# Kernel optimization log

Measured on AMD Instinct MI355X. Metric: run time of the kernel, lower is better.

## Reference

```python
import jax, jax.numpy as jnp
import numpy as np

N_NODES = 100000
N_EDGES = 800000
NODE_F = 32
EDGE_F = 16
HID = 128
EPS = 1e-5


def _bn(h, g, b):
    # BatchNorm1d in training mode: biased batch stats over dim 0
    m = h.mean(axis=0)
    v = jnp.mean((h - m) ** 2, axis=0)
    return (h - m) * jax.lax.rsqrt(v + EPS) * g + b


def _sage(x, src, dst, Wl, bl, Wr):
    # PyG SAGEConv (mean aggr): lin_l(mean_{j->i} x_j) + lin_r(x_i)
    s = jax.ops.segment_sum(x[src], dst, num_segments=N_NODES)
    cnt = jax.ops.segment_sum(jnp.ones((src.shape[0], 1), x.dtype), dst, num_segments=N_NODES)
    mean = s / jnp.maximum(cnt, 1.0)
    return mean @ Wl + bl + x @ Wr


def setup_inputs() -> dict:
    key = jax.random.key(0)
    ks = jax.random.split(key, 32)

    def lin(k, fi, fo):
        return jax.random.normal(k, (fi, fo), jnp.float32) / np.sqrt(fi)

    inp = {
        'x': jax.random.normal(ks[0], (N_NODES, NODE_F), jnp.float32),
        'edge_index': jax.random.randint(ks[1], (2, N_EDGES), 0, N_NODES),
        'edge_attr': jax.random.normal(ks[2], (N_EDGES, EDGE_F), jnp.float32),
        'edge_source': jax.random.randint(ks[3], (N_EDGES,), 0, N_NODES),
        'edge_target': jax.random.randint(ks[4], (N_EDGES,), 0, N_NODES),
        'W1l': lin(ks[5], NODE_F, HID), 'b1': jnp.zeros((HID,), jnp.float32), 'W1r': lin(ks[6], NODE_F, HID),
        'W2l': lin(ks[7], HID, HID), 'b2': jnp.zeros((HID,), jnp.float32), 'W2r': lin(ks[8], HID, HID),
        'bn1_g': jnp.ones((HID,), jnp.float32), 'bn1_b': jnp.zeros((HID,), jnp.float32),
        'bn2_g': jnp.ones((HID,), jnp.float32), 'bn2_b': jnp.zeros((HID,), jnp.float32),
        'We': lin(ks[9], EDGE_F, HID), 'be': jnp.zeros((HID,), jnp.float32),
        'bne_g': jnp.ones((HID,), jnp.float32), 'bne_b': jnp.zeros((HID,), jnp.float32),
        'Wm1': lin(ks[10], 3 * HID, HID), 'bm1': jnp.zeros((HID,), jnp.float32),
        'bnm_g': jnp.ones((HID,), jnp.float32), 'bnm_b': jnp.zeros((HID,), jnp.float32),
        'Wm2': lin(ks[11], HID, HID // 2), 'bm2': jnp.zeros((HID // 2,), jnp.float32),
        'Wm3': lin(ks[12], HID // 2, 1), 'bm3': jnp.zeros((1,), jnp.float32),
    }
    return inp


def reference(x, edge_index, edge_attr, edge_source, edge_target,
              W1l, b1, W1r, W2l, b2, W2r, bn1_g, bn1_b, bn2_g, bn2_b,
              We, be, bne_g, bne_b, Wm1, bm1, bnm_g, bnm_b, Wm2, bm2, Wm3, bm3):
    src, dst = edge_index[0], edge_index[1]
    h = jax.nn.relu(_bn(_sage(x, src, dst, W1l, b1, W1r), bn1_g, bn1_b))  # dropout = identity (eval)
    h = jax.nn.relu(_bn(_sage(h, src, dst, W2l, b2, W2r), bn2_g, bn2_b))
    ef = _bn(jax.nn.relu(edge_attr @ We + be), bne_g, bne_b)  # Linear->ReLU->BN->Dropout(id)
    z = jnp.concatenate([h[edge_source], h[edge_target], ef], axis=1)  # [E, 3*HID]
    z = _bn(jax.nn.relu(z @ Wm1 + bm1), bnm_g, bnm_b)
    z = jax.nn.relu(z @ Wm2 + bm2)
    return (z @ Wm3 + bm3).squeeze(-1)
```

## Files before the change

kernel.cpp:

```cpp
#include <hip/hip_runtime.h>
#include <hip/hip_bf16.h>

#define NN 100000
#define NE 800000
#define SCAN_NB 98

typedef __attribute__((ext_vector_type(8))) short bf16x8;
typedef __attribute__((ext_vector_type(4))) float f32x4;

__device__ __forceinline__ short f2b(float f) {
    unsigned u = __float_as_uint(f);
    unsigned r = (u + 0x7fffu + ((u >> 16) & 1u)) >> 16;
    return (short)r;
}
__device__ __forceinline__ float b2f(short s) {
    return __uint_as_float(((unsigned)(unsigned short)s) << 16);
}

__global__ __launch_bounds__(256) void k_hist(const int* __restrict__ ei, int* __restrict__ deg)
{
    int e = blockIdx.x * 256 + threadIdx.x;
    if (e < NE) atomicAdd(&deg[ei[NE + e]], 1);
}

__global__ __launch_bounds__(1024) void k_scan_a(const int* __restrict__ deg,
    int* __restrict__ tmp, int* __restrict__ bsum)
{
    __shared__ int sh[1024];
    int t = threadIdx.x, b = blockIdx.x;
    int idx = b * 1024 + t;
    int v = (idx < NN) ? deg[idx] : 0;
    sh[t] = v;
    __syncthreads();
    for (int ofs = 1; ofs < 1024; ofs <<= 1) {
        int u = (t >= ofs) ? sh[t - ofs] : 0;
        __syncthreads();
        sh[t] += u;
        __syncthreads();
    }
    if (idx < NN) tmp[idx] = sh[t] - v;
    if (t == 1023) bsum[b] = sh[1023];
}

__global__ void k_scan_b(const int* __restrict__ bsum, int* __restrict__ boff,
    int* __restrict__ rowptr)
{
    if (threadIdx.x == 0) {
        int acc = 0;
        for (int i = 0; i < SCAN_NB; i++) { boff[i] = acc; acc += bsum[i]; }
        rowptr[NN] = acc;
    }
}

__global__ __launch_bounds__(1024) void k_scan_c(const int* __restrict__ tmp,
    const int* __restrict__ boff, int* __restrict__ rowptr, int* __restrict__ wp)
{
    int b = blockIdx.x, t = threadIdx.x;
    int idx = b * 1024 + t;
    if (idx < NN) {
        int v = boff[b] + tmp[idx];
        rowptr[idx] = v; wp[idx] = v;
    }
}

__global__ __launch_bounds__(256) void k_scatter(const int* __restrict__ ei,
    int* __restrict__ wp, int* __restrict__ elist)
{
    int e = blockIdx.x * 256 + threadIdx.x;
    if (e < NE) {
        int d = ei[NE + e];
        int pos = atomicAdd(&wp[d], 1);
        elist[pos] = ei[e];
    }
}

__global__ __launch_bounds__(256) void k_gagg1(const float* __restrict__ x,
    const int* __restrict__ rowptr, const int* __restrict__ elist, float* __restrict__ meanX)
{
    int n = blockIdx.x * 8 + (threadIdx.x >> 5);
    int j = threadIdx.x & 31;
    int b = rowptr[n], e = rowptr[n + 1];
    float acc = 0.f;
    for (int i = b; i < e; i++) {
        int s = elist[i];
        acc += x[(size_t)s * 32 + j];
    }
    float inv = (e > b) ? 1.0f / (float)(e - b) : 1.0f;
    meanX[(size_t)n * 32 + j] = acc * inv;
}

__global__ __launch_bounds__(256) void k_gagg2(const short* __restrict__ h1b,
    const int* __restrict__ rowptr, const int* __restrict__ elist,
    const float* __restrict__ sc1, const float* __restrict__ sh1, short* __restrict__ m2b)
{
    int n = blockIdx.x * 8 + (threadIdx.x >> 5);
    int c0 = (threadIdx.x & 31) * 4;
    float sc[4], sh[4];
    #pragma unroll
    for (int i = 0; i < 4; i++) { sc[i] = sc1[c0 + i]; sh[i] = sh1[c0 + i]; }
    int b = rowptr[n], e = rowptr[n + 1];
    float acc[4] = {0.f, 0.f, 0.f, 0.f};
    for (int i = b; i < e; i++) {
        int s = elist[i];
        ushort4 u = *(const ushort4*)(h1b + (size_t)s * 128 + c0);
        acc[0] += fmaxf(b2f((short)u.x) * sc[0] + sh[0], 0.f);
        acc[1] += fmaxf(b2f((short)u.y) * sc[1] + sh[1], 0.f);
        acc[2] += fmaxf(b2f((short)u.z) * sc[2] + sh[2], 0.f);
        acc[3] += fmaxf(b2f((short)u.w) * sc[3] + sh[3], 0.f);
    }
    float inv = (e > b) ? 1.0f / (float)(e - b) : 1.0f;
    ushort4 o;
    o.x = (unsigned short)f2b(acc[0] * inv);
    o.y = (unsigned short)f2b(acc[1] * inv);
    o.z = (unsigned short)f2b(acc[2] * inv);
    o.w = (unsigned short)f2b(acc[3] * inv);
    *(ushort4*)(m2b + (size_t)n * 128 + c0) = o;
}

__global__ __launch_bounds__(256) void k_node_l1(
    const float* __restrict__ meanX, const float* __restrict__ x,
    const float* __restrict__ Wl, const float* __restrict__ Wr,
    const float* __restrict__ bias,
    short* __restrict__ outp, float* __restrict__ ssum, float* __restrict__ ssq)
{
    __shared__ __align__(16) float sWl[32][128];
    __shared__ __align__(16) float sWr[32][128];
    __shared__ __align__(16) float sA[32][36];
    __shared__ __align__(16) float sB[32][36];
    __shared__ float red[2][128], red2[2][128];
    int tid = threadIdx.x;
    int j = tid & 127, rg = tid >> 7;
    int r0 = blockIdx.x * 32;

    for (int f = tid * 4; f < 4096; f += 1024) {
        *(float4*)((float*)sWl + f) = *(const float4*)(Wl + f);
        *(float4*)((float*)sWr + f) = *(const float4*)(Wr + f);
    }
    {
        int r = tid >> 3, c = (tid & 7) * 4;
        *(float4*)(&sA[r][c]) = *(const float4*)(meanX + (size_t)(r0 + r) * 32 + c);
        *(float4*)(&sB[r][c]) = *(const float4*)(x + (size_t)(r0 + r) * 32 + c);
    }
    __syncthreads();

    float acc[16];
    #pragma unroll
    for (int r = 0; r < 16; r++) acc[r] = 0.0f;
    int rb = rg * 16;
    #pragma unroll
    for (int kq = 0; kq < 8; kq++) {
        int k = kq * 4;
        float wl0 = sWl[k][j], wl1 = sWl[k+1][j], wl2 = sWl[k+2][j], wl3 = sWl[k+3][j];
        float wr0 = sWr[k][j], wr1 = sWr[k+1][j], wr2 = sWr[k+2][j], wr3 = sWr[k+3][j];
        #pragma unroll
        for (int r = 0; r < 16; r++) {
            float4 a = *(float4*)(&sA[rb + r][k]);
            float4 b = *(float4*)(&sB[rb + r][k]);
            acc[r] += a.x*wl0 + a.y*wl1 + a.z*wl2 + a.w*wl3
                    + b.x*wr0 + b.y*wr1 + b.z*wr2 + b.w*wr3;
        }
    }
    float bj = bias[j];
    float s1 = 0.0f, s2 = 0.0f;
    #pragma unroll
    for (int r = 0; r < 16; r++) {
        float v = acc[r] + bj;
        outp[(size_t)(r0 + rb + r) * 128 + j] = f2b(v);
        s1 += v; s2 += v * v;
    }
    red[rg][j] = s1; red2[rg][j] = s2;
    __syncthreads();
    if (rg == 0) {
        atomicAdd(&ssum[j], red[0][j] + red[1][j]);
        atomicAdd(&ssq[j],  red2[0][j] + red2[1][j]);
    }
}

__global__ __launch_bounds__(256) void k_node_l2m(
    const short* __restrict__ m2b, const short* __restrict__ h1b,
    const float* __restrict__ sc1, const float* __restrict__ sh1,
    const short* __restrict__ W2cT, const float* __restrict__ bias,
    short* __restrict__ h2b, float* __restrict__ ssum, float* __restrict__ ssq)
{
    __shared__ __align__(16) short sK[32][264];
    __shared__ float sRed[2][128];
    __shared__ float sS[128], sH[128];
    const int tid = threadIdx.x;
    const int wave = tid >> 6, lane = tid & 63, quad = lane >> 4, ln = lane & 15;
    const int waveM = wave >> 1, waveN = wave & 1;
    const int colbase = 64 * waveN, row16 = 16 * waveM;
    if (tid < 128) { sS[tid] = sc1[tid]; sH[tid] = sh1[tid]; sRed[0][tid] = 0.f; sRed[1][tid] = 0.f; }

    bf16x8 bW[4][8];
    #pragma unroll
    for (int nt = 0; nt < 4; nt++)
        #pragma unroll
        for (int kk = 0; kk < 8; kk++)
            bW[nt][kk] = *(const bf16x8*)(W2cT + (size_t)(colbase + nt * 16 + ln) * 256 + kk * 32 + quad * 8);
    float bc[4];
    #pragma unroll
    for (int nt = 0; nt < 4; nt++) bc[nt] = bias[colbase + nt * 16 + ln];

    float s1[4] = {0,0,0,0}, s2[4] = {0,0,0,0};
    f32x4 zero = {0.f, 0.f, 0.f, 0.f};
    __syncthreads();

    for (int t = blockIdx.x; t < NN / 32; t += gridDim.x) {
        int r0 = t * 32;
        __syncthreads();
        {
            int r = tid >> 3, seg = tid & 7;
            if (seg < 4) {
                const bf16x8* src = (const bf16x8*)(m2b + (size_t)(r0 + r) * 128 + seg * 32);
                bf16x8* dst = (bf16x8*)(&sK[r][seg * 32]);
                dst[0] = src[0]; dst[1] = src[1]; dst[2] = src[2]; dst[3] = src[3];
            } else {
                int c0 = (seg - 4) * 32;
                const short* src = h1b + (size_t)(r0 + r) * 128 + c0;
                short tmp[32];
                #pragma unroll
                for (int i = 0; i < 32; i++)
                    tmp[i] = f2b(fmaxf(b2f(src[i]) * sS[c0 + i] + sH[c0 + i], 0.f));
                bf16x8* dst = (bf16x8*)(&sK[r][128 + c0]);
                dst[0] = *(bf16x8*)(tmp); dst[1] = *(bf16x8*)(tmp + 8);
                dst[2] = *(bf16x8*)(tmp + 16); dst[3] = *(bf16x8*)(tmp + 24);
            }
        }
        __syncthreads();
        f32x4 acc[4] = {zero, zero, zero, zero};
        #pragma unroll
        for (int kk = 0; kk < 8; kk++) {
            bf16x8 a = *(const bf16x8*)(&sK[row16 + ln][kk * 32 + quad * 8]);
            #pragma unroll
            for (int nt = 0; nt < 4; nt++)
                acc[nt] = __builtin_amdgcn_mfma_f32_16x16x32_bf16(a, bW[nt][kk], acc[nt], 0, 0, 0);
        }
        #pragma unroll
        for (int nt = 0; nt < 4; nt++) {
            int col = colbase + nt * 16 + ln;
            #pragma unroll
            for (int r = 0; r < 4; r++) {
                float v = acc[nt][r] + bc[nt];
                h2b[(size_t)(r0 + row16 + quad * 4 + r) * 128 + col] = f2b(v);
                s1[nt] += v; s2[nt] += v * v;
            }
        }
    }
    #pragma unroll
    for (int nt = 0; nt < 4; nt++) {
        float a1 = s1[nt], a2 = s2[nt];
        a1 += __shfl_down(a1, 32); a1 += __shfl_down(a1, 16);
        a2 += __shfl_down(a2, 32); a2 += __shfl_down(a2, 16);
        if (quad == 0) {
            atomicAdd(&sRed[0][colbase + nt * 16 + ln], a1);
            atomicAdd(&sRed[1][colbase + nt * 16 + ln], a2);
        }
    }
    __syncthreads();
    if (tid < 128) {
        atomicAdd(&ssum[tid], sRed[0][tid]);
        atomicAdd(&ssq[tid],  sRed[1][tid]);
    }
}

__global__ void k_bn_fin(const float* __restrict__ ssum, const float* __restrict__ ssq,
    const float* __restrict__ g, const float* __restrict__ b, float count,
    float* __restrict__ scale, float* __restrict__ shift)
{
    int j = threadIdx.x;
    float m = ssum[j] / count;
    float var = ssq[j] / count - m * m;
    float rs = rsqrtf(var + 1e-5f);
    float sc = g[j] * rs;
    scale[j] = sc;
    shift[j] = b[j] - m * sc;
}

__global__ void k_prep(const float* __restrict__ We, const float* __restrict__ Wm1,
                       const float* __restrict__ W2l, const float* __restrict__ W2r,
                       short* __restrict__ WteT, short* __restrict__ WmsT,
                       short* __restrict__ WmdT, short* __restrict__ W2cT)
{
    int j = threadIdx.x;
    int b = blockIdx.x;
    if (b == 0) {
        for (int k = 0; k < 32; k++)
            WteT[j * 32 + k] = (k < 16) ? f2b(We[k * 128 + j]) : (short)0;
    } else if (b == 1) {
        for (int k = 0; k < 128; k++) WmsT[j * 128 + k] = f2b(Wm1[k * 128 + j]);
    } else if (b == 2) {
        for (int k = 0; k < 128; k++) WmdT[j * 128 + k] = f2b(Wm1[(128 + k) * 128 + j]);
    } else if (b == 3) {
        for (int k = 0; k < 128; k++) W2cT[j * 256 + k] = f2b(W2l[k * 128 + j]);
    } else {
        for (int k = 0; k < 128; k++) W2cT[j * 256 + 128 + k] = f2b(W2r[k * 128 + j]);
    }
}

__global__ void k_fold_e(const float* __restrict__ ssum, const float* __restrict__ ssq,
    const float* __restrict__ g, const float* __restrict__ b,
    const float* __restrict__ Wm1, const float* __restrict__ bm1,
    short* __restrict__ W1pT, float* __restrict__ bm1p)
{
    __shared__ float sa[128], sc[128];
    int tid = threadIdx.x;
    float m = ssum[tid] / (float)NE;
    float var = ssq[tid] / (float)NE - m * m;
    float rs = rsqrtf(var + 1e-5f);
    float a = g[tid] * rs;
    sa[tid] = a; sc[tid] = b[tid] - m * a;
    __syncthreads();
    float acc = bm1[tid];
    for (int k = 0; k < 128; k++) {
        float w = Wm1[(256 + k) * 128 + tid];
        W1pT[tid * 128 + k] = f2b(sa[k] * w);
        acc += sc[k] * w;
    }
    bm1p[tid] = acc;
}

__global__ void k_fold_m(const float* __restrict__ ssum, const float* __restrict__ ssq,
    const float* __restrict__ g, const float* __restrict__ b,
    const float* __restrict__ Wm2, const float* __restrict__ bm2,
    short* __restrict__ W2pT, float* __restrict__ b2p)
{
    __shared__ float sa[128], sc[128];
    int tid = threadIdx.x;
    float m = ssum[tid] / (float)NE;
    float var = ssq[tid] / (float)NE - m * m;
    float rs = rsqrtf(var + 1e-5f);
    float a = g[tid] * rs;
    sa[tid] = a; sc[tid] = b[tid] - m * a;
    __syncthreads();
    if (tid < 64) {
        float acc = bm2[tid];
        for (int k = 0; k < 128; k++) {
            float w = Wm2[k * 64 + tid];
            W2pT[tid * 128 + k] = f2b(sa[k] * w);
            acc += sc[k] * w;
        }
        b2p[tid] = acc;
    }
}

__global__ __launch_bounds__(256) void k_proj_mfma(
    const short* __restrict__ h2b, const float* __restrict__ sc2, const float* __restrict__ sh2,
    const short* __restrict__ WT0, const short* __restrict__ WT1,
    short* __restrict__ C0, short* __restrict__ C1)
{
    __shared__ __align__(16) short sA[32][136];
    __shared__ float sS[128], sH[128];
    const int tid = threadIdx.x;
    const int wave = tid >> 6, lane = tid & 63, quad = lane >> 4, ln = lane & 15;
    const int waveM = wave >> 1, waveN = wave & 1;
    const int colbase = 64 * waveN, row16 = 16 * waveM;
    const int half = (blockIdx.x >= 640) ? 1 : 0;
    const short* WT = half ? WT1 : WT0;
    short* C = half ? C1 : C0;
    const int b0 = blockIdx.x - half * 640;
    if (tid < 128) { sS[tid] = sc2[tid]; sH[tid] = sh2[tid]; }
    bf16x8 bW[4][4];
    #pragma unroll
    for (int nt = 0; nt < 4; nt++)
        #pragma unroll
        for (int kk = 0; kk < 4; kk++)
            bW[nt][kk] = *(const bf16x8*)(WT + (colbase + nt * 16 + ln) * 128 + kk * 32 + quad * 8);
    f32x4 zero = {0.f, 0.f, 0.f, 0.f};
    __syncthreads();
    for (int t = b0; t < NN / 32; t += 640) {
        int r0 = t * 32;
        __syncthreads();
        {
            int r = tid >> 3, c0 = (tid & 7) * 16;
            const short* p = h2b + (size_t)(r0 + r) * 128 + c0;
            short tmp[16];
            #pragma unroll
            for (int i = 0; i < 16; i++)
                tmp[i] = f2b(fmaxf(b2f(p[i]) * sS[c0 + i] + sH[c0 + i], 0.f));
            *(bf16x8*)(&sA[r][c0])     = *(bf16x8*)tmp;
            *(bf16x8*)(&sA[r][c0 + 8]) = *(bf16x8*)(tmp + 8);
        }
        __syncthreads();
        f32x4 acc[4] = {zero, zero, zero, zero};
        #pragma unroll
        for (int kk = 0; kk < 4; kk++) {
            bf16x8 a = *(const bf16x8*)(&sA[row16 + ln][kk * 32 + quad * 8]);
            #pragma unroll
            for (int nt = 0; nt < 4; nt++)
                acc[nt] = __builtin_amdgcn_mfma_f32_16x16x32_bf16(a, bW[nt][kk], acc[nt], 0, 0, 0);
        }
        #pragma unroll
        for (int nt = 0; nt < 4; nt++) {
            int col = colbase + nt * 16 + ln;
            #pragma unroll
            for (int r = 0; r < 4; r++)
                C[(size_t)(r0 + row16 + quad * 4 + r) * 128 + col] = f2b(acc[nt][r]);
        }
    }
}

template<int MODE, bool STOREV = false>
__global__ __launch_bounds__(256) void k_edge_mfma(
    const float* __restrict__ ea,
    const short* __restrict__ WteT, const float* __restrict__ be,
    const short* __restrict__ W1pT, const float* __restrict__ bm1p,
    const short* __restrict__ hs, const short* __restrict__ hd,
    const int* __restrict__ esrc, const int* __restrict__ etgt,
    const short* __restrict__ W2pT, const float* __restrict__ b2p,
    const float* __restrict__ Wm3, const float* __restrict__ bm3,
    float* __restrict__ ssum, float* __restrict__ ssq,
    short* __restrict__ vbuf, float* __restrict__ outp)
{
    __shared__ __align__(16) short sT[32][136];
    __shared__ __align__(16) float sSum[32][132];
    __shared__ float sRed[2][128];
    __shared__ __align__(16) short sW2[64][136];
    __shared__ float sZ[32][69];
    __shared__ float sW3[64];

    const int tid = threadIdx.x;
    const int wave = tid >> 6, lane = tid & 63;
    const int quad = lane >> 4, ln = lane & 15;
    const int waveM = wave >> 1, waveN = wave & 1;
    const int colbase = 64 * waveN, row16 = 16 * waveM;

    if (MODE < 2) {
        if (tid < 128) { sRed[0][tid] = 0.f; sRed[1][tid] = 0.f; }
    }
    if (MODE >= 2) {
        int q = tid >> 2, kb = (tid & 3) * 32;
        const bf16x8* src = (const bf16x8*)(W2pT + q * 128 + kb);
        bf16x8* dst = (bf16x8*)(&sW2[q][kb]);
        dst[0] = src[0]; dst[1] = src[1]; dst[2] = src[2]; dst[3] = src[3];
        if (tid < 64) sW3[tid] = Wm3[tid];
    }

    bf16x8 bWe[4], bW1[4][4];
    if (MODE <= 2) {
        #pragma unroll
        for (int nt = 0; nt < 4; nt++) {
            bWe[nt] = *(const bf16x8*)(WteT + (colbase + nt * 16 + ln) * 32 + quad * 8);
            if (MODE >= 1) {
                #pragma unroll
                for (int kk = 0; kk < 4; kk++)
                    bW1[nt][kk] = *(const bf16x8*)(W1pT + (colbase + nt * 16 + ln) * 128 + kk * 32 + quad * 8);
            }
        }
    }
    float bec[4], bmc[4];
    #pragma unroll
    for (int nt = 0; nt < 4; nt++) {
        bec[nt] = (MODE <= 2) ? be[colbase + nt * 16 + ln] : 0.f;
        bmc[nt] = (MODE == 1 || MODE == 2) ? bm1p[colbase + nt * 16 + ln] : 0.f;
    }
    float b2c[2] = {0.f, 0.f};
    if (MODE >= 2) { b2c[0] = b2p[32 * waveN + ln]; b2c[1] = b2p[32 * waveN + 16 + ln]; }
    float bm3v = (MODE >= 2) ? bm3[0] : 0.f;

    const int srow = tid >> 4;
    const int scol = (tid & 15) * 8;

    float s1[4] = {0,0,0,0}, s2[4] = {0,0,0,0};
    f32x4 zero = {0.f, 0.f, 0.f, 0.f};
    __syncthreads();

    if constexpr (MODE == 1) {
        const int G = gridDim.x;
        const int NT = NE / 32;
        bf16x8 gA = {}, gB = {}, gC = {}, gD = {};
        int i1sA = 0, i1tA = 0, i1sB = 0, i1tB = 0;
        float4 fe0 = {0,0,0,0}, fe1 = {0,0,0,0};

        int t = blockIdx.x;
        if (t < NT) {
            const int e0 = t * 32;
            int s0 = esrc[e0 + srow],      q0 = etgt[e0 + srow];
            int s1i = esrc[e0 + srow + 16], q1 = etgt[e0 + srow + 16];
            gA = *(const bf16x8*)(hs + (size_t)s0 * 128 + scol);
            gB = *(const bf16x8*)(hd + (size_t)q0 * 128 + scol);
            gC = *(const bf16x8*)(hs + (size_t)s1i * 128 + scol);
            gD = *(const bf16x8*)(hd + (size_t)q1 * 128 + scol);
            int t1 = t + G;
            if (t1 < NT) {
                const int e1 = t1 * 32;
                i1sA = esrc[e1 + srow];      i1tA = etgt[e1 + srow];
                i1sB = esrc[e1 + srow + 16]; i1tB = etgt[e1 + srow + 16];
            }
            if (quad < 2) {
                const float* p = ea + (size_t)(e0 + row16 + ln) * 16 + quad * 8;
                fe0 = *(const float4*)p; fe1 = *(const float4*)(p + 4);
            }
        }

        for (; t < NT; t += G) {
            const int e0 = t * 32;

            bf16x8 aE;
            #pragma unroll
            for (int i = 0; i < 8; i++) aE[i] = 0;
            if (quad < 2) {
                aE[0]=f2b(fe0.x); aE[1]=f2b(fe0.y); aE[2]=f2b(fe0.z); aE[3]=f2b(fe0.w);
                aE[4]=f2b(fe1.x); aE[5]=f2b(fe1.y); aE[6]=f2b(fe1.z); aE[7]=f2b(fe1.w);
            }
            f32x4 tacc[4];
            #pragma unroll
            for (int nt = 0; nt < 4; nt++)
                tacc[nt] = __builtin_amdgcn_mfma_f32_16x16x32_bf16(aE, bWe[nt], zero, 0, 0, 0);

            __syncthreads();

            #pragma unroll
            for (int nt = 0; nt < 4; nt++) {
                int col = colbase + nt * 16 + ln;
                #pragma unroll
                for (int r = 0; r < 4; r++)
                    sT[row16 + quad * 4 + r][col] = f2b(fmaxf(tacc[nt][r] + bec[nt], 0.f));
            }
            {
                f32x4 a0, a1, b0, b1;
                #pragma unroll
                for (int i = 0; i < 4; i++) {
                    a0[i] = b2f(gA[i])     + b2f(gB[i]);
                    a1[i] = b2f(gA[i + 4]) + b2f(gB[i + 4]);
                    b0[i] = b2f(gC[i])     + b2f(gD[i]);
                    b1[i] = b2f(gC[i + 4]) + b2f(gD[i + 4]);
                }
                *(f32x4*)(&sSum[srow][scol])          = a0;
                *(f32x4*)(&sSum[srow][scol + 4])      = a1;
                *(f32x4*)(&sSum[srow + 16][scol])     = b0;
                *(f32x4*)(&sSum[srow + 16][scol + 4]) = b1;
            }
            {
                int t1 = t + G;
                if (t1 < NT) {
                    gA = *(const bf16x8*)(hs + (size_t)i1sA * 128 + scol);
                    gB = *(const bf16x8*)(hd + (size_t)i1tA * 128 + scol);
                    gC = *(const bf16x8*)(hs + (size_t)i1sB * 128 + scol);
                    gD = *(const bf16x8*)(hd + (size_t)i1tB * 128 + scol);
                    int t2 = t1 + G;
                    if (t2 < NT) {
                        const int e2 = t2 * 32;
                        i1sA = esrc[e2 + srow];      i1tA = etgt[e2 + srow];
                        i1sB = esrc[e2 + srow + 16]; i1tB = etgt[e2 + srow + 16];
                    }
                    if (quad < 2) {
                        const float* p = ea + (size_t)(t1 * 32 + row16 + ln) * 16 + quad * 8;
                        fe0 = *(const float4*)p; fe1 = *(const float4*)(p + 4);
                    }
                }
            }
            __syncthreads();

            f32x4 uacc[4] = {zero, zero, zero, zero};
            #pragma unroll
            for (int kk = 0; kk < 4; kk++) {
                bf16x8 aU = *(const bf16x8*)(&sT[row16 + ln][kk * 32 + quad * 8]);
                #pragma unroll
                for (int nt = 0; nt < 4; nt++)
                    uacc[nt] = __builtin_amdgcn_mfma_f32_16x16x32_bf16(aU, bW1[nt][kk], uacc[nt], 0, 0, 0);
            }
            #pragma unroll
            for (int nt = 0; nt < 4; nt++) {
                int col = colbase + nt * 16 + ln;
                #pragma unroll
                for (int r = 0; r < 4; r++) {
                    float v = uacc[nt][r] + bmc[nt] + sSum[row16 + quad * 4 + r][col];
                    v = fmaxf(v, 0.f);
                    s1[nt] += v; s2[nt] += v * v;
                    if constexpr (STOREV)
                        vbuf[(size_t)(e0 + row16 + quad * 4 + r) * 128 + col] = f2b(v);
                }
            }
        }
    } else {

    for (int t = blockIdx.x; t < NE / 32; t += gridDim.x) {
        const int e0 = t * 32;

        if (MODE == 3) {
            f32x4 vacc[2] = {zero, zero};
            #pragma unroll
            for (int kk = 0; kk < 4; kk++) {
                bf16x8 aV = *(const bf16x8*)(vbuf + (size_t)(e0 + row16 + ln) * 128 + kk * 32 + quad * 8);
                #pragma unroll
                for (int n2 = 0; n2 < 2; n2++) {
                    bf16x8 bV = *(const bf16x8*)(&sW2[32 * waveN + n2 * 16 + ln][kk * 32 + quad * 8]);
                    vacc[n2] = __builtin_amdgcn_mfma_f32_16x16x32_bf16(aV, bV, vacc[n2], 0, 0, 0);
                }
            }
            __syncthreads();
            #pragma unroll
            for (int n2 = 0; n2 < 2; n2++) {
                int col2 = 32 * waveN + n2 * 16 + ln;
                #pragma unroll
                for (int r = 0; r < 4; r++)
                    sZ[row16 + quad * 4 + r][col2] = fmaxf(vacc[n2][r] + b2c[n2], 0.f);
            }
            __syncthreads();
            {
                int row = wave * 8 + (lane >> 3);
                int ks  = (lane & 7) * 8;
                float o = 0.f;
                #pragma unroll
                for (int k2 = 0; k2 < 8; k2++)
                    o += sZ[row][ks + k2] * sW3[ks + k2];
                o += __shfl_xor(o, 1);
                o += __shfl_xor(o, 2);
                o += __shfl_xor(o, 4);
                if ((lane & 7) == 0) outp[e0 + row] = o + bm3v;
            }
            continue;
        }

        int isA = 0, itA = 0, isB = 0, itB = 0;
        if (MODE == 2) {
            isA = esrc[e0 + srow];      itA = etgt[e0 + srow];
            isB = esrc[e0 + srow + 16]; itB = etgt[e0 + srow + 16];
        }

        bf16x8 aE;
        #pragma unroll
        for (int i = 0; i < 8; i++) aE[i] = 0;
        if (quad < 2) {
            const float* p = ea + (size_t)(e0 + row16 + ln) * 16 + quad * 8;
            float4 f0 = *(const float4*)p, f1 = *(const float4*)(p + 4);
            aE[0]=f2b(f0.x); aE[1]=f2b(f0.y); aE[2]=f2b(f0.z); aE[3]=f2b(f0.w);
            aE[4]=f2b(f1.x); aE[5]=f2b(f1.y); aE[6]=f2b(f1.z); aE[7]=f2b(f1.w);
        }
        f32x4 tacc[4];
        #pragma unroll
        for (int nt = 0; nt < 4; nt++)
            tacc[nt] = __builtin_amdgcn_mfma_f32_16x16x32_bf16(aE, bWe[nt], zero, 0, 0, 0);

        if (MODE == 0) {
            #pragma unroll
            for (int nt = 0; nt < 4; nt++)
                #pragma unroll
                for (int r = 0; r < 4; r++) {
                    float v = fmaxf(tacc[nt][r] + bec[nt], 0.f);
                    s1[nt] += v; s2[nt] += v * v;
                }
            continue;
        }

        __syncthreads();
        {
            bf16x8 gA = *(const bf16x8*)(hs + (size_t)isA * 128 + scol);
            bf16x8 gB = *(const bf16x8*)(hd + (size_t)itA * 128 + scol);
            bf16x8 gC = *(const bf16x8*)(hs + (size_t)isB * 128 + scol);
            bf16x8 gD = *(const bf16x8*)(hd + (size_t)itB * 128 + scol);
            #pragma unroll
            for (int nt = 0; nt < 4; nt++) {
                int col = colbase + nt * 16 + ln;
                #pragma unroll
                for (int r = 0; r < 4; r++)
                    sT[row16 + quad * 4 + r][col] = f2b(fmaxf(tacc[nt][r] + bec[nt], 0.f));
            }
            f32x4 a0, a1, b0, b1;
            #pragma unroll
            for (int i = 0; i < 4; i++) {
                a0[i] = b2f(gA[i])     + b2f(gB[i]);
                a1[i] = b2f(gA[i + 4]) + b2f(gB[i + 4]);
                b0[i] = b2f(gC[i])     + b2f(gD[i]);
                b1[i] = b2f(gC[i + 4]) + b2f(gD[i + 4]);
            }
            *(f32x4*)(&sSum[srow][scol])          = a0;
            *(f32x4*)(&sSum[srow][scol + 4])      = a1;
            *(f32x4*)(&sSum[srow + 16][scol])     = b0;
            *(f32x4*)(&sSum[srow + 16][scol + 4]) = b1;
        }
        __syncthreads();

        f32x4 uacc[4] = {zero, zero, zero, zero};
        #pragma unroll
        for (int kk = 0; kk < 4; kk++) {
            bf16x8 aU = *(const bf16x8*)(&sT[row16 + ln][kk * 32 + quad * 8]);
            #pragma unroll
            for (int nt = 0; nt < 4; nt++)
                uacc[nt] = __builtin_amdgcn_mfma_f32_16x16x32_bf16(aU, bW1[nt][kk], uacc[nt], 0, 0, 0);
        }

        {
            __syncthreads();
            #pragma unroll
            for (int nt = 0; nt < 4; nt++) {
                int col = colbase + nt * 16 + ln;
                #pragma unroll
                for (int r = 0; r < 4; r++) {
                    float v = uacc[nt][r] + bmc[nt] + sSum[row16 + quad * 4 + r][col];
                    sT[row16 + quad * 4 + r][col] = f2b(fmaxf(v, 0.f));
                }
            }
            __syncthreads();
            f32x4 vacc[2] = {zero, zero};
            #pragma unroll
            for (int kk = 0; kk < 4; kk++) {
                bf16x8 aV = *(const bf16x8*)(&sT[row16 + ln][kk * 32 + quad * 8]);
                #pragma unroll
                for (int n2 = 0; n2 < 2; n2++) {
                    bf16x8 bV = *(const bf16x8*)(&sW2[32 * waveN + n2 * 16 + ln][kk * 32 + quad * 8]);
                    vacc[n2] = __builtin_amdgcn_mfma_f32_16x16x32_bf16(aV, bV, vacc[n2], 0, 0, 0);
                }
            }
            #pragma unroll
            for (int n2 = 0; n2 < 2; n2++) {
                int col2 = 32 * waveN + n2 * 16 + ln;
                #pragma unroll
                for (int r = 0; r < 4; r++)
                    sZ[row16 + quad * 4 + r][col2] = fmaxf(vacc[n2][r] + b2c[n2], 0.f);
            }
            __syncthreads();
            {
                int row = wave * 8 + (lane >> 3);
                int ks  = (lane & 7) * 8;
                float o = 0.f;
                #pragma unroll
                for (int k2 = 0; k2 < 8; k2++)
                    o += sZ[row][ks + k2] * sW3[ks + k2];
                o += __shfl_xor(o, 1);
                o += __shfl_xor(o, 2);
                o += __shfl_xor(o, 4);
                if ((lane & 7) == 0) outp[e0 + row] = o + bm3v;
            }
        }
    }

    }

    if (MODE < 2) {
        #pragma unroll
        for (int nt = 0; nt < 4; nt++) {
            float a1 = s1[nt], a2 = s2[nt];
            a1 += __shfl_down(a1, 32); a1 += __shfl_down(a1, 16);
            a2 += __shfl_down(a2, 32); a2 += __shfl_down(a2, 16);
            if (quad == 0) {
                atomicAdd(&sRed[0][colbase + nt * 16 + ln], a1);
                atomicAdd(&sRed[1][colbase + nt * 16 + ln], a2);
            }
        }
        __syncthreads();
        if (tid < 128) {
            atomicAdd(&ssum[tid], sRed[0][tid]);
            atomicAdd(&ssq[tid],  sRed[1][tid]);
        }
    }
}

extern "C" void kernel_launch(void* const* d_in, const int* in_sizes, int n_in,
                              void* d_out, int out_size, void* d_ws, size_t ws_size,
                              hipStream_t stream) {
    const float* x     = (const float*)d_in[0];
    const int*   ei    = (const int*)  d_in[1];
    const float* eattr = (const float*)d_in[2];
    const int*   esrc  = (const int*)  d_in[3];
    const int*   etgt  = (const int*)  d_in[4];
    const float* W1l = (const float*)d_in[5];  const float* b1 = (const float*)d_in[6];
    const float* W1r = (const float*)d_in[7];
    const float* W2l = (const float*)d_in[8];  const float* b2 = (const float*)d_in[9];
    const float* W2r = (const float*)d_in[10];
    const float* bn1_g = (const float*)d_in[11]; const float* bn1_b = (const float*)d_in[12];
    const float* bn2_g = (const float*)d_in[13]; const float* bn2_b = (const float*)d_in[14];
    const float* We  = (const float*)d_in[15]; const float* be  = (const float*)d_in[16];
    const float* bne_g = (const float*)d_in[17]; const float* bne_b = (const float*)d_in[18];
    const float* Wm1 = (const float*)d_in[19]; const float* bm1 = (const float*)d_in[20];
    const float* bnm_g = (const float*)d_in[21]; const float* bnm_b = (const float*)d_in[22];
    const float* Wm2 = (const float*)d_in[23]; const float* bm2 = (const float*)d_in[24];
    const float* Wm3 = (const float*)d_in[25]; const float* bm3 = (const float*)d_in[26];
    float* out = (float*)d_out;

    char* base = (char*)d_ws;
    size_t o = 0;
    auto A = [&](size_t bytes) { char* p = base + o; o = (o + bytes + 255) & ~(size_t)255; return p; };
    short* hsb   = (short*)A((size_t)NN * 128 * 2);
    short* hdb   = (short*)A((size_t)NN * 128 * 2);
    int*   deg   = (int*)  A((size_t)NN * 4);
    int*   rowptr= (int*)  A((size_t)(NN + 1) * 4);
    int*   wp    = (int*)  A((size_t)NN * 4);
    int*   elist = (int*)  A((size_t)NE * 4);
    float* st    = (float*)A(1024 * 4);
    int*   bsum  = (int*)  A(SCAN_NB * 4);
    int*   boff  = (int*)  A(SCAN_NB * 4);
    float* sc1   = (float*)A(512); float* sh1 = (float*)A(512);
    float* sc2   = (float*)A(512); float* sh2 = (float*)A(512);
    float* bm1p  = (float*)A(512); float* b2p = (float*)A(256);
    short* WteT  = (short*)A(128 * 32 * 2);
    short* W1pT  = (short*)A(128 * 128 * 2);
    short* WmsT  = (short*)A(128 * 128 * 2);
    short* WmdT  = (short*)A(128 * 128 * 2);
    short* W2pT  = (short*)A(64 * 128 * 2);
    short* W2cT  = (short*)A(128 * 256 * 2);
    size_t chain = o;
    float* meanX = (float*)A((size_t)NN * 32 * 4);
    short* h1b   = (short*)A((size_t)NN * 128 * 2);
    short* m2b   = (short*)A((size_t)NN * 128 * 2);
    short* h2b   = (short*)A((size_t)NN * 128 * 2);
    int*   stmp  = (int*)meanX;
    short* vbuf  = (short*)(base + chain);
    bool storev = ws_size >= chain + (size_t)NE * 128 * 2;

    hipMemsetAsync(deg, 0, (size_t)NN * 4, stream);
    hipMemsetAsync(st, 0, 1024 * 4, stream);

    k_prep<<<5, 128, 0, stream>>>(We, Wm1, W2l, W2r, WteT, WmsT, WmdT, W2cT);
    k_hist<<<(NE + 255) / 256, 256, 0, stream>>>(ei, deg);
    k_scan_a<<<SCAN_NB, 1024, 0, stream>>>(deg, stmp, bsum);
    k_scan_b<<<1, 64, 0, stream>>>(bsum, boff, rowptr);
    k_scan_c<<<SCAN_NB, 1024, 0, stream>>>(stmp, boff, rowptr, wp);
    k_scatter<<<(NE + 255) / 256, 256, 0, stream>>>(ei, wp, elist);

    k_edge_mfma<0><<<1024, 256, 0, stream>>>(eattr, WteT, be, W1pT, bm1p, hsb, hdb,
        esrc, etgt, W2pT, b2p, Wm3, bm3, st + 512, st + 640, nullptr, out);
    k_fold_e<<<1, 128, 0, stream>>>(st + 512, st + 640, bne_g, bne_b, Wm1, bm1, W1pT, bm1p);

    k_gagg1<<<NN / 8, 256, 0, stream>>>(x, rowptr, elist, meanX);
    k_node_l1<<<NN / 32, 256, 0, stream>>>(meanX, x, W1l, W1r, b1, h1b, st + 0, st + 128);
    k_bn_fin<<<1, 128, 0, stream>>>(st + 0, st + 128, bn1_g, bn1_b, (float)NN, sc1, sh1);

    k_gagg2<<<NN / 8, 256, 0, stream>>>(h1b, rowptr, elist, sc1, sh1, m2b);
    k_node_l2m<<<640, 256, 0, stream>>>(m2b, h1b, sc1, sh1, W2cT, b2, h2b, st + 256, st + 384);
    k_bn_fin<<<1, 128, 0, stream>>>(st + 256, st + 384, bn2_g, bn2_b, (float)NN, sc2, sh2);

    k_proj_mfma<<<1280, 256, 0, stream>>>(h2b, sc2, sh2, WmsT, WmdT, hsb, hdb);

    if (storev)
        k_edge_mfma<1, true><<<1280, 256, 0, stream>>>(eattr, WteT, be, W1pT, bm1p, hsb, hdb,
            esrc, etgt, W2pT, b2p, Wm3, bm3, st + 768, st + 896, vbuf, out);
    else
        k_edge_mfma<1, false><<<1280, 256, 0, stream>>>(eattr, WteT, be, W1pT, bm1p, hsb, hdb,
            esrc, etgt, W2pT, b2p, Wm3, bm3, st + 768, st + 896, nullptr, out);
    k_fold_m<<<1, 128, 0, stream>>>(st + 768, st + 896, bnm_g, bnm_b, Wm2, bm2, W2pT, b2p);

    if (storev)
        k_edge_mfma<3><<<2048, 256, 0, stream>>>(eattr, WteT, be, W1pT, bm1p, hsb, hdb,
            esrc, etgt, W2pT, b2p, Wm3, bm3, nullptr, nullptr, vbuf, out);
    else
        k_edge_mfma<2><<<1280, 256, 0, stream>>>(eattr, WteT, be, W1pT, bm1p, hsb, hdb,
            esrc, etgt, W2pT, b2p, Wm3, bm3, nullptr, nullptr, nullptr, out);
}
```

Baseline: 813.6 us.

## Unroll gather loops, prefetch next tile in edge kernels, retune grid sizes

The neighbor-gather loops in both SAGE aggregation kernels are unrolled by four so several independent row loads are in flight at once. The edge-attribute stats pass (mode 0) and the final MLP pass over stored activations (mode 3) are split into dedicated loops that load the next tile into registers before computing the current one. Grid sizes for several kernels change, with matching stride changes in the projection kernel. This hides gather and global-load latency at the cost of more registers and a different float summation order.

```diff
diff --git a/kernel.cpp b/kernel.cpp
--- a/kernel.cpp
+++ b/kernel.cpp
@@ -81,10 +81,16 @@
     int j = threadIdx.x & 31;
     int b = rowptr[n], e = rowptr[n + 1];
     float acc = 0.f;
-    for (int i = b; i < e; i++) {
-        int s = elist[i];
-        acc += x[(size_t)s * 32 + j];
-    }
+    int i = b;
+    for (; i + 4 <= e; i += 4) {
+        int s0 = elist[i], s1 = elist[i + 1], s2 = elist[i + 2], s3 = elist[i + 3];
+        float a0 = x[(size_t)s0 * 32 + j];
+        float a1 = x[(size_t)s1 * 32 + j];
+        float a2 = x[(size_t)s2 * 32 + j];
+        float a3 = x[(size_t)s3 * 32 + j];
+        acc += (a0 + a1) + (a2 + a3);
+    }
+    for (; i < e; i++) acc += x[(size_t)elist[i] * 32 + j];
     float inv = (e > b) ? 1.0f / (float)(e - b) : 1.0f;
     meanX[(size_t)n * 32 + j] = acc * inv;
 }
@@ -100,7 +106,23 @@
     for (int i = 0; i < 4; i++) { sc[i] = sc1[c0 + i]; sh[i] = sh1[c0 + i]; }
     int b = rowptr[n], e = rowptr[n + 1];
     float acc[4] = {0.f, 0.f, 0.f, 0.f};
-    for (int i = b; i < e; i++) {
+    int i = b;
+    for (; i + 4 <= e; i += 4) {
+        int s0 = elist[i], s1 = elist[i + 1], s2 = elist[i + 2], s3 = elist[i + 3];
+        ushort4 u0 = *(const ushort4*)(h1b + (size_t)s0 * 128 + c0);
+        ushort4 u1 = *(const ushort4*)(h1b + (size_t)s1 * 128 + c0);
+        ushort4 u2 = *(const ushort4*)(h1b + (size_t)s2 * 128 + c0);
+        ushort4 u3 = *(const ushort4*)(h1b + (size_t)s3 * 128 + c0);
+        acc[0] += fmaxf(b2f((short)u0.x) * sc[0] + sh[0], 0.f) + fmaxf(b2f((short)u1.x) * sc[0] + sh[0], 0.f)
+                + fmaxf(b2f((short)u2.x) * sc[0] + sh[0], 0.f) + fmaxf(b2f((short)u3.x) * sc[0] + sh[0], 0.f);
+        acc[1] += fmaxf(b2f((short)u0.y) * sc[1] + sh[1], 0.f) + fmaxf(b2f((short)u1.y) * sc[1] + sh[1], 0.f)
+                + fmaxf(b2f((short)u2.y) * sc[1] + sh[1], 0.f) + fmaxf(b2f((short)u3.y) * sc[1] + sh[1], 0.f);
+        acc[2] += fmaxf(b2f((short)u0.z) * sc[2] + sh[2], 0.f) + fmaxf(b2f((short)u1.z) * sc[2] + sh[2], 0.f)
+                + fmaxf(b2f((short)u2.z) * sc[2] + sh[2], 0.f) + fmaxf(b2f((short)u3.z) * sc[2] + sh[2], 0.f);
+        acc[3] += fmaxf(b2f((short)u0.w) * sc[3] + sh[3], 0.f) + fmaxf(b2f((short)u1.w) * sc[3] + sh[3], 0.f)
+                + fmaxf(b2f((short)u2.w) * sc[3] + sh[3], 0.f) + fmaxf(b2f((short)u3.w) * sc[3] + sh[3], 0.f);
+    }
+    for (; i < e; i++) {
         int s = elist[i];
         ushort4 u = *(const ushort4*)(h1b + (size_t)s * 128 + c0);
         acc[0] += fmaxf(b2f((short)u.x) * sc[0] + sh[0], 0.f);
@@ -354,10 +376,10 @@
     const int wave = tid >> 6, lane = tid & 63, quad = lane >> 4, ln = lane & 15;
     const int waveM = wave >> 1, waveN = wave & 1;
     const int colbase = 64 * waveN, row16 = 16 * waveM;
-    const int half = (blockIdx.x >= 640) ? 1 : 0;
+    const int half = (blockIdx.x >= 512) ? 1 : 0;
     const short* WT = half ? WT1 : WT0;
     short* C = half ? C1 : C0;
-    const int b0 = blockIdx.x - half * 640;
+    const int b0 = blockIdx.x - half * 512;
     if (tid < 128) { sS[tid] = sc2[tid]; sH[tid] = sh2[tid]; }
     bf16x8 bW[4][4];
     #pragma unroll
@@ -367,7 +389,7 @@
             bW[nt][kk] = *(const bf16x8*)(WT + (colbase + nt * 16 + ln) * 128 + kk * 32 + quad * 8);
     f32x4 zero = {0.f, 0.f, 0.f, 0.f};
     __syncthreads();
-    for (int t = b0; t < NN / 32; t += 640) {
+    for (int t = b0; t < NN / 32; t += 512) {
         int r0 = t * 32;
         __syncthreads();
         {
@@ -572,20 +594,74 @@
                 }
             }
         }
-    } else {
-
-    for (int t = blockIdx.x; t < NE / 32; t += gridDim.x) {
-        const int e0 = t * 32;
-
-        if (MODE == 3) {
+    } else if constexpr (MODE == 0) {
+        const int G = gridDim.x;
+        const int NT = NE / 32;
+        float4 fe0 = {0,0,0,0}, fe1 = {0,0,0,0};
+        int t = blockIdx.x;
+        if (t < NT && quad < 2) {
+            const float* p = ea + (size_t)(t * 32 + row16 + ln) * 16 + quad * 8;
+            fe0 = *(const float4*)p; fe1 = *(const float4*)(p + 4);
+        }
+        for (; t < NT; t += G) {
+            bf16x8 aE;
+            #pragma unroll
+            for (int i = 0; i < 8; i++) aE[i] = 0;
+            if (quad < 2) {
+                aE[0]=f2b(fe0.x); aE[1]=f2b(fe0.y); aE[2]=f2b(fe0.z); aE[3]=f2b(fe0.w);
+                aE[4]=f2b(fe1.x); aE[5]=f2b(fe1.y); aE[6]=f2b(fe1.z); aE[7]=f2b(fe1.w);
+            }
+            int t1 = t + G;
+            if (t1 < NT && quad < 2) {
+                const float* p = ea + (size_t)(t1 * 32 + row16 + ln) * 16 + quad * 8;
+                fe0 = *(const float4*)p; fe1 = *(const float4*)(p + 4);
+            }
+            f32x4 tacc[4];
+            #pragma unroll
+            for (int nt = 0; nt < 4; nt++)
+                tacc[nt] = __builtin_amdgcn_mfma_f32_16x16x32_bf16(aE, bWe[nt], zero, 0, 0, 0);
+            #pragma unroll
+            for (int nt = 0; nt < 4; nt++)
+                #pragma unroll
+                for (int r = 0; r < 4; r++) {
+                    float v = fmaxf(tacc[nt][r] + bec[nt], 0.f);
+                    s1[nt] += v; s2[nt] += v * v;
+                }
+        }
+    } else if constexpr (MODE == 3) {
+        const int G = gridDim.x;
+        const int NT = NE / 32;
+        bf16x8 aV0 = {}, aV1 = {}, aV2 = {}, aV3 = {};
+        int t = blockIdx.x;
+        if (t < NT) {
+            const short* p = vbuf + (size_t)(t * 32 + row16 + ln) * 128 + quad * 8;
+            aV0 = *(const bf16x8*)(p);
+            aV1 = *(const bf16x8*)(p + 32);
+            aV2 = *(const bf16x8*)(p + 64);
+            aV3 = *(const bf16x8*)(p + 96);
+        }
+        for (; t < NT; t += G) {
+            const int e0 = t * 32;
             f32x4 vacc[2] = {zero, zero};
             #pragma unroll
-            for (int kk = 0; kk < 4; kk++) {
-                bf16x8 aV = *(const bf16x8*)(vbuf + (size_t)(e0 + row16 + ln) * 128 + kk * 32 + quad * 8);
-                #pragma unroll
-                for (int n2 = 0; n2 < 2; n2++) {
-                    bf16x8 bV = *(const bf16x8*)(&sW2[32 * waveN + n2 * 16 + ln][kk * 32 + quad * 8]);
-                    vacc[n2] = __builtin_amdgcn_mfma_f32_16x16x32_bf16(aV, bV, vacc[n2], 0, 0, 0);
+            for (int n2 = 0; n2 < 2; n2++) {
+                bf16x8 bV0 = *(const bf16x8*)(&sW2[32 * waveN + n2 * 16 + ln][0 * 32 + quad * 8]);
+                bf16x8 bV1 = *(const bf16x8*)(&sW2[32 * waveN + n2 * 16 + ln][1 * 32 + quad * 8]);
+                bf16x8 bV2 = *(const bf16x8*)(&sW2[32 * waveN + n2 * 16 + ln][2 * 32 + quad * 8]);
+                bf16x8 bV3 = *(const bf16x8*)(&sW2[32 * waveN + n2 * 16 + ln][3 * 32 + quad * 8]);
+                vacc[n2] = __builtin_amdgcn_mfma_f32_16x16x32_bf16(aV0, bV0, vacc[n2], 0, 0, 0);
+                vacc[n2] = __builtin_amdgcn_mfma_f32_16x16x32_bf16(aV1, bV1, vacc[n2], 0, 0, 0);
+                vacc[n2] = __builtin_amdgcn_mfma_f32_16x16x32_bf16(aV2, bV2, vacc[n2], 0, 0, 0);
+                vacc[n2] = __builtin_amdgcn_mfma_f32_16x16x32_bf16(aV3, bV3, vacc[n2], 0, 0, 0);
+            }
+            {
+                int t1 = t + G;
+                if (t1 < NT) {
+                    const short* p = vbuf + (size_t)(t1 * 32 + row16 + ln) * 128 + quad * 8;
+                    aV0 = *(const bf16x8*)(p);
+                    aV1 = *(const bf16x8*)(p + 32);
+                    aV2 = *(const bf16x8*)(p + 64);
+                    aV3 = *(const bf16x8*)(p + 96);
                 }
             }
             __syncthreads();
@@ -609,14 +685,13 @@
                 o += __shfl_xor(o, 4);
                 if ((lane & 7) == 0) outp[e0 + row] = o + bm3v;
             }
-            continue;
-        }
-
-        int isA = 0, itA = 0, isB = 0, itB = 0;
-        if (MODE == 2) {
-            isA = esrc[e0 + srow];      itA = etgt[e0 + srow];
-            isB = esrc[e0 + srow + 16]; itB = etgt[e0 + srow + 16];
-        }
+        }
+    } else {
+    for (int t = blockIdx.x; t < NE / 32; t += gridDim.x) {
+        const int e0 = t * 32;
+
+        int isA = esrc[e0 + srow],      itA = etgt[e0 + srow];
+        int isB = esrc[e0 + srow + 16], itB = etgt[e0 + srow + 16];
 
         bf16x8 aE;
         #pragma unroll
@@ -632,17 +707,6 @@
         for (int nt = 0; nt < 4; nt++)
             tacc[nt] = __builtin_amdgcn_mfma_f32_16x16x32_bf16(aE, bWe[nt], zero, 0, 0, 0);
 
-        if (MODE == 0) {
-            #pragma unroll
-            for (int nt = 0; nt < 4; nt++)
-                #pragma unroll
-                for (int r = 0; r < 4; r++) {
-                    float v = fmaxf(tacc[nt][r] + bec[nt], 0.f);
-                    s1[nt] += v; s2[nt] += v * v;
-                }
-            continue;
-        }
-
         __syncthreads();
         {
             bf16x8 gA = *(const bf16x8*)(hs + (size_t)isA * 128 + scol);
@@ -680,51 +744,48 @@
                 uacc[nt] = __builtin_amdgcn_mfma_f32_16x16x32_bf16(aU, bW1[nt][kk], uacc[nt], 0, 0, 0);
         }
 
+        __syncthreads();
+        #pragma unroll
+        for (int nt = 0; nt < 4; nt++) {
+            int col = colbase + nt * 16 + ln;
+            #pragma unroll
+            for (int r = 0; r < 4; r++) {
+                float v = uacc[nt][r] + bmc[nt] + sSum[row16 + quad * 4 + r][col];
+                sT[row16 + quad * 4 + r][col] = f2b(fmaxf(v, 0.f));
+            }
+        }
+        __syncthreads();
+        f32x4 vacc[2] = {zero, zero};
+        #pragma unroll
+        for (int kk = 0; kk < 4; kk++) {
+            bf16x8 aV = *(const bf16x8*)(&sT[row16 + ln][kk * 32 + quad * 8]);
+            #pragma unroll
+            for (int n2 = 0; n2 < 2; n2++) {
+                bf16x8 bV = *(const bf16x8*)(&sW2[32 * waveN + n2 * 16 + ln][kk * 32 + quad * 8]);
+                vacc[n2] = __builtin_amdgcn_mfma_f32_16x16x32_bf16(aV, bV, vacc[n2], 0, 0, 0);
+            }
+        }
+        #pragma unroll
+        for (int n2 = 0; n2 < 2; n2++) {
+            int col2 = 32 * waveN + n2 * 16 + ln;
+            #pragma unroll
+            for (int r = 0; r < 4; r++)
+                sZ[row16 + quad * 4 + r][col2] = fmaxf(vacc[n2][r] + b2c[n2], 0.f);
+        }
+        __syncthreads();
         {
-            __syncthreads();
-            #pragma unroll
-            for (int nt = 0; nt < 4; nt++) {
-                int col = colbase + nt * 16 + ln;
-                #pragma unroll
-                for (int r = 0; r < 4; r++) {
-                    float v = uacc[nt][r] + bmc[nt] + sSum[row16 + quad * 4 + r][col];
-                    sT[row16 + quad * 4 + r][col] = f2b(fmaxf(v, 0.f));
-                }
-            }
-            __syncthreads();
-            f32x4 vacc[2] = {zero, zero};
-            #pragma unroll
-            for (int kk = 0; kk < 4; kk++) {
-                bf16x8 aV = *(const bf16x8*)(&sT[row16 + ln][kk * 32 + quad * 8]);
-                #pragma unroll
-                for (int n2 = 0; n2 < 2; n2++) {
-                    bf16x8 bV = *(const bf16x8*)(&sW2[32 * waveN + n2 * 16 + ln][kk * 32 + quad * 8]);
-                    vacc[n2] = __builtin_amdgcn_mfma_f32_16x16x32_bf16(aV, bV, vacc[n2], 0, 0, 0);
-                }
-            }
-            #pragma unroll
-            for (int n2 = 0; n2 < 2; n2++) {
-                int col2 = 32 * waveN + n2 * 16 + ln;
-                #pragma unroll
-                for (int r = 0; r < 4; r++)
-                    sZ[row16 + quad * 4 + r][col2] = fmaxf(vacc[n2][r] + b2c[n2], 0.f);
-            }
-            __syncthreads();
-            {
-                int row = wave * 8 + (lane >> 3);
-                int ks  = (lane & 7) * 8;
-                float o = 0.f;
-                #pragma unroll
-                for (int k2 = 0; k2 < 8; k2++)
-                    o += sZ[row][ks + k2] * sW3[ks + k2];
-                o += __shfl_xor(o, 1);
-                o += __shfl_xor(o, 2);
-                o += __shfl_xor(o, 4);
-                if ((lane & 7) == 0) outp[e0 + row] = o + bm3v;
-            }
-        }
-    }
-
+            int row = wave * 8 + (lane >> 3);
+            int ks  = (lane & 7) * 8;
+            float o = 0.f;
+            #pragma unroll
+            for (int k2 = 0; k2 < 8; k2++)
+                o += sZ[row][ks + k2] * sW3[ks + k2];
+            o += __shfl_xor(o, 1);
+            o += __shfl_xor(o, 2);
+            o += __shfl_xor(o, 4);
+            if ((lane & 7) == 0) outp[e0 + row] = o + bm3v;
+        }
+    }
     }
 
     if (MODE < 2) {
@@ -808,7 +869,7 @@
     k_scan_c<<<SCAN_NB, 1024, 0, stream>>>(stmp, boff, rowptr, wp);
     k_scatter<<<(NE + 255) / 256, 256, 0, stream>>>(ei, wp, elist);
 
-    k_edge_mfma<0><<<1024, 256, 0, stream>>>(eattr, WteT, be, W1pT, bm1p, hsb, hdb,
+    k_edge_mfma<0><<<2048, 256, 0, stream>>>(eattr, WteT, be, W1pT, bm1p, hsb, hdb,
         esrc, etgt, W2pT, b2p, Wm3, bm3, st + 512, st + 640, nullptr, out);
     k_fold_e<<<1, 128, 0, stream>>>(st + 512, st + 640, bne_g, bne_b, Wm1, bm1, W1pT, bm1p);
 
@@ -817,23 +878,23 @@
     k_bn_fin<<<1, 128, 0, stream>>>(st + 0, st + 128, bn1_g, bn1_b, (float)NN, sc1, sh1);
 
     k_gagg2<<<NN / 8, 256, 0, stream>>>(h1b, rowptr, elist, sc1, sh1, m2b);
-    k_node_l2m<<<640, 256, 0, stream>>>(m2b, h1b, sc1, sh1, W2cT, b2, h2b, st + 256, st + 384);
+    k_node_l2m<<<512, 256, 0, stream>>>(m2b, h1b, sc1, sh1, W2cT, b2, h2b, st + 256, st + 384);
     k_bn_fin<<<1, 128, 0, stream>>>(st + 256, st + 384, bn2_g, bn2_b, (float)NN, sc2, sh2);
 
-    k_proj_mfma<<<1280, 256, 0, stream>>>(h2b, sc2, sh2, WmsT, WmdT, hsb, hdb);
+    k_proj_mfma<<<1024, 256, 0, stream>>>(h2b, sc2, sh2, WmsT, WmdT, hsb, hdb);
 
     if (storev)
-        k_edge_mfma<1, true><<<1280, 256, 0, stream>>>(eattr, WteT, be, W1pT, bm1p, hsb, hdb,
+        k_edge_mfma<1, true><<<1024, 256, 0, stream>>>(eattr, WteT, be, W1pT, bm1p, hsb, hdb,
             esrc, etgt, W2pT, b2p, Wm3, bm3, st + 768, st + 896, vbuf, out);
     else
-        k_edge_mfma<1, false><<<1280, 256, 0, stream>>>(eattr, WteT, be, W1pT, bm1p, hsb, hdb,
+        k_edge_mfma<1, false><<<1024, 256, 0, stream>>>(eattr, WteT, be, W1pT, bm1p, hsb, hdb,
             esrc, etgt, W2pT, b2p, Wm3, bm3, st + 768, st + 896, nullptr, out);
     k_fold_m<<<1, 128, 0, stream>>>(st + 768, st + 896, bnm_g, bnm_b, Wm2, bm2, W2pT, b2p);
 
     if (storev)
-        k_edge_mfma<3><<<2048, 256, 0, stream>>>(eattr, WteT, be, W1pT, bm1p, hsb, hdb,
+        k_edge_mfma<3><<<1536, 256, 0, stream>>>(eattr, WteT, be, W1pT, bm1p, hsb, hdb,
             esrc, etgt, W2pT, b2p, Wm3, bm3, nullptr, nullptr, vbuf, out);
     else
-        k_edge_mfma<2><<<1280, 256, 0, stream>>>(eattr, WteT, be, W1pT, bm1p, hsb, hdb,
+        k_edge_mfma<2><<<1024, 256, 0, stream>>>(eattr, WteT, be, W1pT, bm1p, hsb, hdb,
             esrc, etgt, W2pT, b2p, Wm3, bm3, nullptr, nullptr, nullptr, out);
 }
```

Result: faster. 752.3 us (-7.5%).
